# Optimization experiments

Hardware: AMD Instinct MI355X
Metric: run time of the kernel (lower is better)

## Reference

```python
import jax, jax.numpy as jnp
import numpy as np

D_MODEL = 1024
NUM_HEADS = 16
D_K = D_MODEL // NUM_HEADS
BLOCK_SIZE = 64
SPARSITY_FACTOR = 4


def sparse_mask(seq_len):
    i = jnp.arange(seq_len)[:, None]
    j = jnp.arange(seq_len)[None, :]
    local = jnp.abs(j - i) <= BLOCK_SIZE // 2  # window [i-32, i+32]
    strided = (j % SPARSITY_FACTOR) == (i % SPARSITY_FACTOR)
    return local | strided  # [S, S] bool


def setup_inputs() -> dict:
    key = jax.random.key(0)
    ks = jax.random.split(key, 9)
    s = 1.0 / np.sqrt(D_MODEL)
    x = jax.random.normal(ks[0], (2, 2048, D_MODEL), dtype=jnp.float32)
    Wq = jax.random.normal(ks[1], (D_MODEL, D_MODEL), dtype=jnp.float32) * s
    Wk = jax.random.normal(ks[2], (D_MODEL, D_MODEL), dtype=jnp.float32) * s
    Wv = jax.random.normal(ks[3], (D_MODEL, D_MODEL), dtype=jnp.float32) * s
    Wo = jax.random.normal(ks[4], (D_MODEL, D_MODEL), dtype=jnp.float32) * s
    bq = jax.random.normal(ks[5], (D_MODEL,), dtype=jnp.float32) * 0.01
    bk = jax.random.normal(ks[6], (D_MODEL,), dtype=jnp.float32) * 0.01
    bv = jax.random.normal(ks[7], (D_MODEL,), dtype=jnp.float32) * 0.01
    bo = jax.random.normal(ks[8], (D_MODEL,), dtype=jnp.float32) * 0.01
    return {"x": x, "Wq": Wq, "bq": bq, "Wk": Wk, "bk": bk,
            "Wv": Wv, "bv": bv, "Wo": Wo, "bo": bo}


def reference(x, Wq, bq, Wk, bk, Wv, bv, Wo, bo):
    B, S, _ = x.shape
    # nn.Linear: y = x @ W.T + b
    def heads(W, b):
        return (x @ W.T + b).reshape(B, S, NUM_HEADS, D_K).transpose(0, 2, 1, 3)
    Q = heads(Wq, bq)  # [B,H,S,Dk]
    K = heads(Wk, bk)
    V = heads(Wv, bv)
    scores = jnp.einsum('bhsd,bhtd->bhst', Q, K) / np.sqrt(D_K)  # [B,H,S,S]
    mask = sparse_mask(S)  # [S,S]
    scores = jnp.where(mask[None, None], scores, -jnp.inf)
    probs = jax.nn.softmax(scores, axis=-1)
    out = jnp.einsum('bhst,bhtd->bhsd', probs, V)  # [B,H,S,Dk]
    out = out.transpose(0, 2, 1, 3).reshape(B, S, D_MODEL)
    return out @ Wo.T + bo
```

## Files before the change

### kernel.cpp

```cpp
#include <hip/hip_runtime.h>

typedef unsigned short ushort_t;
typedef __bf16 bf16x8 __attribute__((ext_vector_type(8)));
typedef float  f32x4  __attribute__((ext_vector_type(4)));

#define MFMA16(a,b,c) __builtin_amdgcn_mfma_f32_16x16x32_bf16((a),(b),(c),0,0,0)

__device__ __forceinline__ ushort_t f2bf(float f) {
    union { float f; unsigned u; } x; x.f = f;
    unsigned r = (x.u + 0x7fffu + ((x.u >> 16) & 1u)) >> 16;
    return (ushort_t)r;
}

__device__ __forceinline__ void gload16(const ushort_t* g, char* l) {
    __builtin_amdgcn_global_load_lds(
        (const __attribute__((address_space(1))) unsigned*)g,
        (__attribute__((address_space(3))) unsigned*)l, 16, 0, 0);
}

__global__ void cast_all(const float* __restrict__ x,
                         const float* __restrict__ Wq, const float* __restrict__ Wk,
                         const float* __restrict__ Wv, const float* __restrict__ Wo,
                         ushort_t* __restrict__ xbf, ushort_t* __restrict__ wqkv,
                         ushort_t* __restrict__ wob) {
    int i = blockIdx.x * 256 + threadIdx.x;
    float4 v;
    if (i < 1048576) {
        v = ((const float4*)x)[i];
        ushort4 o;
        o.x = f2bf(v.x); o.y = f2bf(v.y); o.z = f2bf(v.z); o.w = f2bf(v.w);
        ((ushort4*)xbf)[i] = o;
    } else {
        int j = i - 1048576;
        int r = j >> 18, jj = j & 0x3ffff;
        const float* src = (r == 0) ? Wq : (r == 1) ? Wk : (r == 2) ? Wv : Wo;
        v = ((const float4*)src)[jj];
        ushort4 o;
        o.x = f2bf(v.x); o.y = f2bf(v.y); o.z = f2bf(v.z); o.w = f2bf(v.w);
        if (r < 3) ((ushort4*)wqkv)[(size_t)r*262144 + jj] = o;
        else       ((ushort4*)wob)[jj] = o;
    }
}

template<int MODE>
__global__ void gemm_bt(const ushort_t* __restrict__ A,
                        const ushort_t* __restrict__ Bw,
                        const float* __restrict__ b0, const float* __restrict__ b1,
                        const float* __restrict__ b2,
                        void* __restrict__ C0, void* __restrict__ C1,
                        void* __restrict__ C2, void* __restrict__ C3,
                        void* __restrict__ C4)
{
    __shared__ __align__(16) char lds[32768];
    char* As = lds;
    char* Bs = lds + 16384;
    const int tid  = threadIdx.x;
    const int lane = tid & 63;
    const int wid  = tid >> 6;
    const int wrow = wid >> 1;
    const int wcol = wid & 1;
    const int m0 = blockIdx.x * 128;
    const int n0 = blockIdx.y * 128;

    f32x4 acc[4][4] = {};

    #define STAGE(kb)                                                          \
        _Pragma("unroll")                                                      \
        for (int k = 0; k < 4; ++k) {                                          \
            int idx = k*256 + tid;                                             \
            int row = idx >> 3, s = idx & 7;                                   \
            int sc = s ^ (row & 7);                                            \
            gload16(A  + (size_t)(m0+row)*1024 + (kb) + sc*8, As + idx*16);    \
            gload16(Bw + (size_t)(n0+row)*1024 + (kb) + sc*8, Bs + idx*16);    \
        }

    STAGE(0)
    for (int kt = 0; kt < 16; ++kt) {
        __syncthreads();
        #pragma unroll
        for (int ks = 0; ks < 2; ++ks) {
            bf16x8 af[4], bfr[4];
            #pragma unroll
            for (int i = 0; i < 4; ++i) {
                int row = wrow*64 + i*16 + (lane & 15);
                int sl  = ks*4 + (lane >> 4);
                af[i] = *(const bf16x8*)(As + row*128 + ((sl ^ (row & 7)) << 4));
            }
            #pragma unroll
            for (int j = 0; j < 4; ++j) {
                int row = wcol*64 + j*16 + (lane & 15);
                int sl  = ks*4 + (lane >> 4);
                bfr[j] = *(const bf16x8*)(Bs + row*128 + ((sl ^ (row & 7)) << 4));
            }
            #pragma unroll
            for (int i = 0; i < 4; ++i)
                #pragma unroll
                for (int j = 0; j < 4; ++j)
                    acc[i][j] = MFMA16(af[i], bfr[j], acc[i][j]);
        }
        __syncthreads();
        if (kt < 15) STAGE((kt+1)*64)
    }
    #undef STAGE

    #pragma unroll
    for (int i = 0; i < 4; ++i) {
        #pragma unroll
        for (int j = 0; j < 4; ++j) {
            #pragma unroll
            for (int q = 0; q < 4; ++q) {
                int gm = m0 + wrow*64 + i*16 + (lane >> 4)*4 + q;
                int gn = n0 + wcol*64 + j*16 + (lane & 15);
                if (MODE == 1) {
                    ((float*)C0)[(size_t)gm*1024 + gn] = acc[i][j][q] + b0[gn];
                } else {
                    int reg = gn >> 10, nn = gn & 1023;
                    float bias = ((reg == 0) ? b0 : (reg == 1) ? b1 : b2)[nn];
                    float v = acc[i][j][q] + bias;
                    int b = gm >> 11, s = gm & 2047;
                    int h = nn >> 6,  dk = nn & 63;
                    int hh = b*16 + h;
                    ushort_t bv = f2bf(v);
                    if (reg == 0) {
                        ((ushort_t*)C0)[((size_t)hh*2048 + s)*64 + dk] = bv;
                    } else if (reg == 1) {
                        ((ushort_t*)C1)[((size_t)hh*2048 + s)*64 + dk] = bv;
                        ((ushort_t*)C2)[(((size_t)hh*4 + (s & 3))*512 + (s >> 2))*64 + dk] = bv;
                    } else {
                        ((ushort_t*)C3)[((size_t)hh*64 + dk)*2048 + s] = bv;
                        ((ushort_t*)C4)[(((size_t)hh*4 + (s & 3))*64 + dk)*512 + (s >> 2)] = bv;
                    }
                }
            }
        }
    }
}

__global__ __launch_bounds__(256, 2)
void sparse_attn7(const ushort_t* __restrict__ Qg,
                  const ushort_t* __restrict__ Kn,
                  const ushort_t* __restrict__ Kss,
                  const ushort_t* __restrict__ Vtn,
                  const ushort_t* __restrict__ Vts,
                  ushort_t* __restrict__ attn)
{
    __shared__ __align__(16) char Klds[2][8192];
    __shared__ __align__(16) char Vlds[2][8192];
    __shared__ __align__(16) char Ps[8192];
    const int tid  = threadIdx.x;
    const int lane = tid & 63;
    const int w    = tid >> 6;
    const int l15  = lane & 15;
    const int lhi  = lane >> 4;
    const int id2  = (blockIdx.x & 7)*128 + (blockIdx.x >> 3);
    const int bh   = id2 >> 5;
    const int rem  = id2 & 31;
    const int r    = rem >> 3;
    const int g    = rem & 7;
    char* Pw = Ps + w*2048;

    const ushort_t* Kst = Kss + ((size_t)bh*4 + r)*512*64;
    const ushort_t* Vst = Vts + ((size_t)bh*4 + r)*64*512;
    const ushort_t* Knb = Kn  + (size_t)bh*2048*64;
    const ushort_t* Vtb = Vtn + (size_t)bh*64*2048;

    const int bl0 = (g > 0) ? 4*g - 1 : 0;
    const int bl1 = (g < 7) ? 4*g + 4 : 31;
    const int NT  = 8 + (bl1 - bl0 + 1);

    bf16x8 aq[2];
    {
        const ushort_t* qp = Qg + ((size_t)bh*2048 + r + 4*(g*64 + w*16 + l15))*64 + lhi*8;
        aq[0] = *(const bf16x8*)(qp);
        aq[1] = *(const bf16x8*)(qp + 32);
    }

    float tsum[4] = {0.f, 0.f, 0.f, 0.f};
    f32x4 oacc[4] = {};

    #define ASTAGE(t, b)                                                         \
        _Pragma("unroll")                                                        \
        for (int k = 0; k < 2; ++k) {                                            \
            int idx = k*256 + tid;                                               \
            int row = idx >> 3, s = idx & 7;                                     \
            int sc = s ^ (row & 7);                                              \
            if ((t) < 8) {                                                       \
                gload16(Kst + (size_t)((t)*64 + row)*64 + sc*8, &Klds[b][idx*16]); \
                gload16(Vst + (size_t)row*512 + (t)*64 + sc*8, &Vlds[b][idx*16]); \
            } else {                                                             \
                int bl = bl0 + (t) - 8;                                          \
                gload16(Knb + (size_t)(bl*64 + row)*64 + sc*8, &Klds[b][idx*16]); \
                gload16(Vtb + (size_t)row*2048 + bl*64 + sc*8, &Vlds[b][idx*16]); \
            }                                                                    \
        }

    ASTAGE(0, 0)
    int cur = 0;
    for (int t = 0; t < NT; ++t) {
        __syncthreads();
        if (t + 1 < NT) ASTAGE(t + 1, cur ^ 1)
        f32x4 sacc[4] = {};
        #pragma unroll
        for (int ks = 0; ks < 2; ++ks) {
            bf16x8 bk[4];
            #pragma unroll
            for (int n = 0; n < 4; ++n) {
                int row = n*16 + l15;
                int sl  = ks*4 + lhi;
                bk[n] = *(const bf16x8*)(&Klds[cur][row*128 + ((sl ^ (row & 7)) << 4)]);
            }
            #pragma unroll
            for (int n = 0; n < 4; ++n)
                sacc[n] = MFMA16(aq[ks], bk[n], sacc[n]);
        }
        if (t < 8) {
            #pragma unroll
            for (int n = 0; n < 4; ++n) {
                int colb = (n*16 + l15) * 2;
                #pragma unroll
                for (int q = 0; q < 4; ++q) {
                    float p = __expf(sacc[n][q]*0.125f - 16.f);
                    tsum[q] += p;
                    int rowp = lhi*4 + q;
                    *(__bf16*)(Pw + rowp*128 + (colb ^ ((rowp & 7) << 4))) = (__bf16)p;
                }
            }
        } else {
            int bl = bl0 + t - 8;
            bool notstr = ((l15 & 3) != r);
            #pragma unroll
            for (int n = 0; n < 4; ++n) {
                int j = bl*64 + n*16 + l15;
                int colb = (n*16 + l15) * 2;
                #pragma unroll
                for (int q = 0; q < 4; ++q) {
                    int i = r + 4*(g*64 + w*16 + 4*lhi + q);
                    int d = j - i;
                    bool valid = notstr && (d <= 32) && (d >= -32);
                    float sv = valid ? sacc[n][q]*0.125f : -1e30f;
                    float p = __expf(sv - 16.f);
                    tsum[q] += p;
                    int rowp = lhi*4 + q;
                    *(__bf16*)(Pw + rowp*128 + (colb ^ ((rowp & 7) << 4))) = (__bf16)p;
                }
            }
        }
        #pragma unroll
        for (int ks = 0; ks < 2; ++ks) {
            int sl = ks*4 + lhi;
            bf16x8 pf = *(const bf16x8*)(Pw + l15*128 + ((sl ^ (l15 & 7)) << 4));
            #pragma unroll
            for (int d = 0; d < 4; ++d) {
                int rowv = d*16 + l15;
                bf16x8 vf = *(const bf16x8*)(&Vlds[cur][rowv*128 + ((sl ^ (rowv & 7)) << 4)]);
                oacc[d] = MFMA16(pf, vf, oacc[d]);
            }
        }
        cur ^= 1;
    }
    #undef ASTAGE

    const int b = bh >> 4, h = bh & 15;
    f32x4 invv;
    #pragma unroll
    for (int q = 0; q < 4; ++q) {
        float t = tsum[q];
        t += __shfl_xor(t, 1);
        t += __shfl_xor(t, 2);
        t += __shfl_xor(t, 4);
        t += __shfl_xor(t, 8);
        invv[q] = 1.f / t;
    }
    #pragma unroll
    for (int d = 0; d < 4; ++d) {
        f32x4 o = oacc[d] * invv;
        #pragma unroll
        for (int q = 0; q < 4; ++q) {
            int srow = r + 4*(g*64 + w*16 + 4*lhi + q);
            int gr = b*2048 + srow;
            int gc = h*64 + d*16 + l15;
            attn[(size_t)gr*1024 + gc] = f2bf(o[q]);
        }
    }
}

extern "C" void kernel_launch(void* const* d_in, const int* in_sizes, int n_in,
                              void* d_out, int out_size, void* d_ws, size_t ws_size,
                              hipStream_t stream)
{
    const float* x  = (const float*)d_in[0];
    const float* Wq = (const float*)d_in[1];
    const float* bq = (const float*)d_in[2];
    const float* Wk = (const float*)d_in[3];
    const float* bk = (const float*)d_in[4];
    const float* Wv = (const float*)d_in[5];
    const float* bv = (const float*)d_in[6];
    const float* Wo = (const float*)d_in[7];
    const float* bo = (const float*)d_in[8];

    char* ws = (char*)d_ws;
    ushort_t* xbf  = (ushort_t*)(ws);
    ushort_t* wqkv = (ushort_t*)(ws + ((size_t)8  << 20));
    ushort_t* wob  = (ushort_t*)(ws + ((size_t)14 << 20));
    ushort_t* Qb   = (ushort_t*)(ws + ((size_t)16 << 20));
    ushort_t* Kn   = (ushort_t*)(ws + ((size_t)24 << 20));
    ushort_t* Kss  = (ushort_t*)(ws + ((size_t)32 << 20));
    ushort_t* Vtn  = (ushort_t*)(ws + ((size_t)40 << 20));
    ushort_t* Vts  = (ushort_t*)(ws + ((size_t)48 << 20));
    ushort_t* attn = (ushort_t*)(ws + ((size_t)56 << 20));

    cast_all<<<8192, 256, 0, stream>>>(x, Wq, Wk, Wv, Wo, xbf, wqkv, wob);

    gemm_bt<0><<<dim3(32, 24), 256, 0, stream>>>(xbf, wqkv, bq, bk, bv,
                                                 Qb, Kn, Kss, Vtn, Vts);

    sparse_attn7<<<dim3(1024), 256, 0, stream>>>(Qb, Kn, Kss, Vtn, Vts, attn);

    gemm_bt<1><<<dim3(32, 8), 256, 0, stream>>>(attn, wob, bo, nullptr, nullptr,
                                                d_out, nullptr, nullptr, nullptr, nullptr);
}
```

Measured before the change: 109.4 us.

## Double-buffer LDS tiles in bf16 GEMM to overlap loads with MFMA

```diff
diff --git a/kernel.cpp b/kernel.cpp
--- a/kernel.cpp
+++ b/kernel.cpp
@@ -43,17 +43,20 @@
 }
 
 template<int MODE>
-__global__ void gemm_bt(const ushort_t* __restrict__ A,
-                        const ushort_t* __restrict__ Bw,
-                        const float* __restrict__ b0, const float* __restrict__ b1,
-                        const float* __restrict__ b2,
-                        void* __restrict__ C0, void* __restrict__ C1,
-                        void* __restrict__ C2, void* __restrict__ C3,
-                        void* __restrict__ C4)
+__global__ __launch_bounds__(256, 2)
+void gemm_bt(const ushort_t* __restrict__ A,
+             const ushort_t* __restrict__ Bw,
+             const float* __restrict__ b0, const float* __restrict__ b1,
+             const float* __restrict__ b2,
+             void* __restrict__ C0, void* __restrict__ C1,
+             void* __restrict__ C2, void* __restrict__ C3,
+             void* __restrict__ C4)
 {
-    __shared__ __align__(16) char lds[32768];
-    char* As = lds;
-    char* Bs = lds + 16384;
+    __shared__ __align__(16) char lds[65536];
+    char* const As0 = lds;
+    char* const Bs0 = lds + 16384;
+    char* const As1 = lds + 32768;
+    char* const Bs1 = lds + 49152;
     const int tid  = threadIdx.x;
     const int lane = tid & 63;
     const int wid  = tid >> 6;
@@ -64,44 +67,52 @@
 
     f32x4 acc[4][4] = {};
 
-    #define STAGE(kb)                                                          \
+    #define STAGE(dA, dB, kb)                                                  \
         _Pragma("unroll")                                                      \
         for (int k = 0; k < 4; ++k) {                                          \
             int idx = k*256 + tid;                                             \
             int row = idx >> 3, s = idx & 7;                                   \
             int sc = s ^ (row & 7);                                            \
-            gload16(A  + (size_t)(m0+row)*1024 + (kb) + sc*8, As + idx*16);    \
-            gload16(Bw + (size_t)(n0+row)*1024 + (kb) + sc*8, Bs + idx*16);    \
-        }
-
-    STAGE(0)
-    for (int kt = 0; kt < 16; ++kt) {
+            gload16(A  + (size_t)(m0+row)*1024 + (kb) + sc*8, (dA) + idx*16);  \
+            gload16(Bw + (size_t)(n0+row)*1024 + (kb) + sc*8, (dB) + idx*16);  \
+        }
+
+    #define COMPUTE(sA, sB)                                                    \
+        _Pragma("unroll")                                                      \
+        for (int ks = 0; ks < 2; ++ks) {                                       \
+            bf16x8 af[4], bfr[4];                                              \
+            _Pragma("unroll")                                                  \
+            for (int i = 0; i < 4; ++i) {                                      \
+                int row = wrow*64 + i*16 + (lane & 15);                        \
+                int sl  = ks*4 + (lane >> 4);                                  \
+                af[i] = *(const bf16x8*)((sA) + row*128 + ((sl ^ (row & 7)) << 4)); \
+            }                                                                  \
+            _Pragma("unroll")                                                  \
+            for (int j = 0; j < 4; ++j) {                                      \
+                int row = wcol*64 + j*16 + (lane & 15);                        \
+                int sl  = ks*4 + (lane >> 4);                                  \
+                bfr[j] = *(const bf16x8*)((sB) + row*128 + ((sl ^ (row & 7)) << 4)); \
+            }                                                                  \
+            _Pragma("unroll")                                                  \
+            for (int i = 0; i < 4; ++i)                                        \
+                _Pragma("unroll")                                              \
+                for (int j = 0; j < 4; ++j)                                    \
+                    acc[i][j] = MFMA16(af[i], bfr[j], acc[i][j]);              \
+        }
+
+    STAGE(As0, Bs0, 0)
+    __syncthreads();
+    #pragma unroll
+    for (int kt2 = 0; kt2 < 8; ++kt2) {
+        if (2*kt2 + 1 < 16) STAGE(As1, Bs1, (2*kt2+1)*64)
+        COMPUTE(As0, Bs0)
         __syncthreads();
-        #pragma unroll
-        for (int ks = 0; ks < 2; ++ks) {
-            bf16x8 af[4], bfr[4];
-            #pragma unroll
-            for (int i = 0; i < 4; ++i) {
-                int row = wrow*64 + i*16 + (lane & 15);
-                int sl  = ks*4 + (lane >> 4);
-                af[i] = *(const bf16x8*)(As + row*128 + ((sl ^ (row & 7)) << 4));
-            }
-            #pragma unroll
-            for (int j = 0; j < 4; ++j) {
-                int row = wcol*64 + j*16 + (lane & 15);
-                int sl  = ks*4 + (lane >> 4);
-                bfr[j] = *(const bf16x8*)(Bs + row*128 + ((sl ^ (row & 7)) << 4));
-            }
-            #pragma unroll
-            for (int i = 0; i < 4; ++i)
-                #pragma unroll
-                for (int j = 0; j < 4; ++j)
-                    acc[i][j] = MFMA16(af[i], bfr[j], acc[i][j]);
-        }
+        if (2*kt2 + 2 < 16) STAGE(As0, Bs0, (2*kt2+2)*64)
+        COMPUTE(As1, Bs1)
         __syncthreads();
-        if (kt < 15) STAGE((kt+1)*64)
     }
     #undef STAGE
+    #undef COMPUTE
 
     #pragma unroll
     for (int i = 0; i < 4; ++i) {
```

Result: faster. 105.2 us (-3.9%).

## Drop duplicate natural K/V copies and stage QKV epilogue through LDS

Applied to the files above, without the earlier changes.

```diff
diff --git a/kernel.cpp b/kernel.cpp
--- a/kernel.cpp
+++ b/kernel.cpp
@@ -48,8 +48,7 @@
                         const float* __restrict__ b0, const float* __restrict__ b1,
                         const float* __restrict__ b2,
                         void* __restrict__ C0, void* __restrict__ C1,
-                        void* __restrict__ C2, void* __restrict__ C3,
-                        void* __restrict__ C4)
+                        void* __restrict__ C2)
 {
     __shared__ __align__(16) char lds[32768];
     char* As = lds;
@@ -59,6 +58,8 @@
     const int wid  = tid >> 6;
     const int wrow = wid >> 1;
     const int wcol = wid & 1;
+    const int l15  = lane & 15;
+    const int lhi  = lane >> 4;
     const int m0 = blockIdx.x * 128;
     const int n0 = blockIdx.y * 128;
 
@@ -82,14 +83,14 @@
             bf16x8 af[4], bfr[4];
             #pragma unroll
             for (int i = 0; i < 4; ++i) {
-                int row = wrow*64 + i*16 + (lane & 15);
-                int sl  = ks*4 + (lane >> 4);
+                int row = wrow*64 + i*16 + l15;
+                int sl  = ks*4 + lhi;
                 af[i] = *(const bf16x8*)(As + row*128 + ((sl ^ (row & 7)) << 4));
             }
             #pragma unroll
             for (int j = 0; j < 4; ++j) {
-                int row = wcol*64 + j*16 + (lane & 15);
-                int sl  = ks*4 + (lane >> 4);
+                int row = wcol*64 + j*16 + l15;
+                int sl  = ks*4 + lhi;
                 bfr[j] = *(const bf16x8*)(Bs + row*128 + ((sl ^ (row & 7)) << 4));
             }
             #pragma unroll
@@ -103,44 +104,77 @@
     }
     #undef STAGE
 
+    if (MODE == 1) {
+        #pragma unroll
+        for (int i = 0; i < 4; ++i)
+            #pragma unroll
+            for (int j = 0; j < 4; ++j)
+                #pragma unroll
+                for (int q = 0; q < 4; ++q) {
+                    int gm = m0 + wrow*64 + i*16 + lhi*4 + q;
+                    int gn = n0 + wcol*64 + j*16 + l15;
+                    ((float*)C0)[(size_t)gm*1024 + gn] = acc[i][j][q] + b0[gn];
+                }
+        return;
+    }
+
+    const int reg  = n0 >> 10;
+    const int nnw0 = (n0 & 1023) + wcol*64;
+    const int h    = nnw0 >> 6;
+    const int b    = (m0 + wrow*64) >> 11;
+    const int s0w  = (m0 + wrow*64) & 2047;
+    const size_t hh = (size_t)b*16 + h;
+    const float* bp = (reg == 0) ? b0 : (reg == 1) ? b1 : b2;
+    char* Cw = lds + wid*8192;
+
+    if (reg == 2) {
+        #pragma unroll
+        for (int i = 0; i < 4; ++i)
+            #pragma unroll
+            for (int j = 0; j < 4; ++j)
+                #pragma unroll
+                for (int q = 0; q < 4; ++q) {
+                    float v = acc[i][j][q] + bp[nnw0 + j*16 + l15];
+                    int rowl = j*16 + l15;
+                    int cb = (q*16 + i*4 + lhi) * 2;
+                    *(__bf16*)(Cw + rowl*128 + (cb & 15) + ((((cb >> 4)) ^ (rowl & 7)) << 4)) = (__bf16)v;
+                }
+    } else {
+        #pragma unroll
+        for (int i = 0; i < 4; ++i)
+            #pragma unroll
+            for (int j = 0; j < 4; ++j)
+                #pragma unroll
+                for (int q = 0; q < 4; ++q) {
+                    float v = acc[i][j][q] + bp[nnw0 + j*16 + l15];
+                    int rowl = i*16 + lhi*4 + q;
+                    int cb = (j*16 + l15) * 2;
+                    *(__bf16*)(Cw + rowl*128 + (cb & 15) + ((((cb >> 4)) ^ (rowl & 7)) << 4)) = (__bf16)v;
+                }
+    }
+    __syncthreads();
+
+    const int rowr = lane >> 3;
+    const int sl2  = lane & 7;
     #pragma unroll
-    for (int i = 0; i < 4; ++i) {
-        #pragma unroll
-        for (int j = 0; j < 4; ++j) {
-            #pragma unroll
-            for (int q = 0; q < 4; ++q) {
-                int gm = m0 + wrow*64 + i*16 + (lane >> 4)*4 + q;
-                int gn = n0 + wcol*64 + j*16 + (lane & 15);
-                if (MODE == 1) {
-                    ((float*)C0)[(size_t)gm*1024 + gn] = acc[i][j][q] + b0[gn];
-                } else {
-                    int reg = gn >> 10, nn = gn & 1023;
-                    float bias = ((reg == 0) ? b0 : (reg == 1) ? b1 : b2)[nn];
-                    float v = acc[i][j][q] + bias;
-                    int b = gm >> 11, s = gm & 2047;
-                    int h = nn >> 6,  dk = nn & 63;
-                    int hh = b*16 + h;
-                    ushort_t bv = f2bf(v);
-                    if (reg == 0) {
-                        ((ushort_t*)C0)[((size_t)hh*2048 + s)*64 + dk] = bv;
-                    } else if (reg == 1) {
-                        ((ushort_t*)C1)[((size_t)hh*2048 + s)*64 + dk] = bv;
-                        ((ushort_t*)C2)[(((size_t)hh*4 + (s & 3))*512 + (s >> 2))*64 + dk] = bv;
-                    } else {
-                        ((ushort_t*)C3)[((size_t)hh*64 + dk)*2048 + s] = bv;
-                        ((ushort_t*)C4)[(((size_t)hh*4 + (s & 3))*64 + dk)*512 + (s >> 2)] = bv;
-                    }
-                }
-            }
-        }
+    for (int p = 0; p < 8; ++p) {
+        int row = p*8 + rowr;
+        bf16x8 val = *(const bf16x8*)(Cw + row*128 + ((sl2 ^ (row & 7)) << 4));
+        ushort_t* dst;
+        if (reg == 0) {
+            dst = (ushort_t*)C0 + (hh*2048 + s0w + row)*64 + sl2*8;
+        } else if (reg == 1) {
+            dst = (ushort_t*)C1 + ((hh*4 + (row & 3))*512 + (s0w >> 2) + (row >> 2))*64 + sl2*8;
+        } else {
+            dst = (ushort_t*)C2 + ((hh*4 + (sl2 >> 1))*64 + row)*512 + (s0w >> 2) + (sl2 & 1)*8;
+        }
+        *(bf16x8*)dst = val;
     }
 }
 
 __global__ __launch_bounds__(256, 2)
-void sparse_attn7(const ushort_t* __restrict__ Qg,
-                  const ushort_t* __restrict__ Kn,
+void sparse_attn8(const ushort_t* __restrict__ Qg,
                   const ushort_t* __restrict__ Kss,
-                  const ushort_t* __restrict__ Vtn,
                   const ushort_t* __restrict__ Vts,
                   ushort_t* __restrict__ attn)
 {
@@ -159,10 +193,10 @@
     const int g    = rem & 7;
     char* Pw = Ps + w*2048;
 
-    const ushort_t* Kst = Kss + ((size_t)bh*4 + r)*512*64;
-    const ushort_t* Vst = Vts + ((size_t)bh*4 + r)*64*512;
-    const ushort_t* Knb = Kn  + (size_t)bh*2048*64;
-    const ushort_t* Vtb = Vtn + (size_t)bh*64*2048;
+    const ushort_t* Kst0 = Kss + (size_t)bh*4*512*64;
+    const ushort_t* Vts0 = Vts + (size_t)bh*4*64*512;
+    const ushort_t* Kst  = Kst0 + (size_t)r*512*64;
+    const ushort_t* Vst  = Vts0 + (size_t)r*64*512;
 
     const int bl0 = (g > 0) ? 4*g - 1 : 0;
     const int bl1 = (g < 7) ? 4*g + 4 : 31;
@@ -178,20 +212,22 @@
     float tsum[4] = {0.f, 0.f, 0.f, 0.f};
     f32x4 oacc[4] = {};
 
-    #define ASTAGE(t, b)                                                         \
-        _Pragma("unroll")                                                        \
-        for (int k = 0; k < 2; ++k) {                                            \
-            int idx = k*256 + tid;                                               \
-            int row = idx >> 3, s = idx & 7;                                     \
-            int sc = s ^ (row & 7);                                              \
-            if ((t) < 8) {                                                       \
+    #define ASTAGE(t, b)                                                           \
+        _Pragma("unroll")                                                          \
+        for (int k = 0; k < 2; ++k) {                                              \
+            int idx = k*256 + tid;                                                 \
+            int row = idx >> 3, s = idx & 7;                                       \
+            int sc = s ^ (row & 7);                                                \
+            if ((t) < 8) {                                                         \
                 gload16(Kst + (size_t)((t)*64 + row)*64 + sc*8, &Klds[b][idx*16]); \
-                gload16(Vst + (size_t)row*512 + (t)*64 + sc*8, &Vlds[b][idx*16]); \
-            } else {                                                             \
-                int bl = bl0 + (t) - 8;                                          \
-                gload16(Knb + (size_t)(bl*64 + row)*64 + sc*8, &Klds[b][idx*16]); \
-                gload16(Vtb + (size_t)row*2048 + bl*64 + sc*8, &Vlds[b][idx*16]); \
-            }                                                                    \
+                gload16(Vst + (size_t)row*512 + (t)*64 + sc*8, &Vlds[b][idx*16]);  \
+            } else {                                                               \
+                int bl = bl0 + (t) - 8;                                            \
+                gload16(Kst0 + (size_t)((row>>4)*512 + bl*16 + (row&15))*64 + sc*8,\
+                        &Klds[b][idx*16]);                                         \
+                gload16(Vts0 + (size_t)((sc>>1)*64 + row)*512 + bl*16 + (sc&1)*8,  \
+                        &Vlds[b][idx*16]);                                         \
+            }                                                                      \
         }
 
     ASTAGE(0, 0)
@@ -227,16 +263,16 @@
             }
         } else {
             int bl = bl0 + t - 8;
-            bool notstr = ((l15 & 3) != r);
             #pragma unroll
             for (int n = 0; n < 4; ++n) {
-                int j = bl*64 + n*16 + l15;
+                int j = 4*(bl*16 + l15) + n;
                 int colb = (n*16 + l15) * 2;
+                bool nres = (n != r);
                 #pragma unroll
                 for (int q = 0; q < 4; ++q) {
                     int i = r + 4*(g*64 + w*16 + 4*lhi + q);
                     int d = j - i;
-                    bool valid = notstr && (d <= 32) && (d >= -32);
+                    bool valid = nres && (d <= 32) && (d >= -32);
                     float sv = valid ? sacc[n][q]*0.125f : -1e30f;
                     float p = __expf(sv - 16.f);
                     tsum[q] += p;
@@ -303,19 +339,17 @@
     ushort_t* wqkv = (ushort_t*)(ws + ((size_t)8  << 20));
     ushort_t* wob  = (ushort_t*)(ws + ((size_t)14 << 20));
     ushort_t* Qb   = (ushort_t*)(ws + ((size_t)16 << 20));
-    ushort_t* Kn   = (ushort_t*)(ws + ((size_t)24 << 20));
-    ushort_t* Kss  = (ushort_t*)(ws + ((size_t)32 << 20));
-    ushort_t* Vtn  = (ushort_t*)(ws + ((size_t)40 << 20));
-    ushort_t* Vts  = (ushort_t*)(ws + ((size_t)48 << 20));
-    ushort_t* attn = (ushort_t*)(ws + ((size_t)56 << 20));
+    ushort_t* Kss  = (ushort_t*)(ws + ((size_t)24 << 20));
+    ushort_t* Vts  = (ushort_t*)(ws + ((size_t)32 << 20));
+    ushort_t* attn = (ushort_t*)(ws + ((size_t)40 << 20));
 
     cast_all<<<8192, 256, 0, stream>>>(x, Wq, Wk, Wv, Wo, xbf, wqkv, wob);
 
     gemm_bt<0><<<dim3(32, 24), 256, 0, stream>>>(xbf, wqkv, bq, bk, bv,
-                                                 Qb, Kn, Kss, Vtn, Vts);
-
-    sparse_attn7<<<dim3(1024), 256, 0, stream>>>(Qb, Kn, Kss, Vtn, Vts, attn);
+                                                 Qb, Kss, Vts);
+
+    sparse_attn8<<<dim3(1024), 256, 0, stream>>>(Qb, Kss, Vts, attn);
 
     gemm_bt<1><<<dim3(32, 8), 256, 0, stream>>>(attn, wob, bo, nullptr, nullptr,
-                                                d_out, nullptr, nullptr, nullptr, nullptr);
-}
+                                                d_out, nullptr, nullptr);
+}
```

Result: faster. 94.50 us (-13.6%).
